# Optimization experiments

Measured on AMD Instinct MI355X. Metric: run time of the kernel, lower is better.

The kernel has to match this reference:

```python
import jax, jax.numpy as jnp
import numpy as np

N = 50000      # number of nodes (rows of edge_embeddings)
E = 800000     # number of edges
D = 256        # edge_dim
TOPK = 50


def setup_inputs() -> dict:
    key = jax.random.key(0)
    k1, k2, k3, k4, k5, k6 = jax.random.split(key, 6)
    edge_embeddings = jax.random.normal(k1, (N, D), dtype=jnp.float32)
    edge_index = jax.random.randint(k2, (2, E), 0, N, dtype=jnp.int64)
    # PyTorch nn.Linear default init: U(-1/sqrt(fan_in), 1/sqrt(fan_in))
    s1 = 1.0 / np.sqrt(2 * D)
    s2 = 1.0 / np.sqrt(D)
    W1 = jax.random.uniform(k3, (2 * D, D), jnp.float32, -s1, s1)
    b1 = jax.random.uniform(k4, (D,), jnp.float32, -s1, s1)
    W2 = jax.random.uniform(k5, (D, 1), jnp.float32, -s2, s2)
    b2 = jax.random.uniform(k6, (1,), jnp.float32, -s2, s2)
    return {"edge_embeddings": edge_embeddings, "W1": W1, "b1": b1,
            "W2": W2, "b2": b2, "edge_index": edge_index, "top_k": TOPK}


def reference(edge_embeddings, W1, b1, W2, b2, edge_index, top_k):
    src, dst = edge_index[0], edge_index[1]           # [E]
    valid = src < dst                                  # original keeps only i<j pairs
    # gather + concat: [E, 2D]
    pair_emb = jnp.concatenate([edge_embeddings[src], edge_embeddings[dst]], axis=-1)
    h = jax.nn.relu(pair_emb @ W1 + b1)                # [E, D]
    score = jax.nn.sigmoid(h @ W2 + b2)[:, 0]          # [E], in (0,1)
    # invalid edges get score -1 (< any sigmoid output) so topk picks only valid ones
    masked = jnp.where(valid, score, jnp.float32(-1.0))
    top_scores, top_idx = jax.lax.top_k(masked, top_k)
    top_pairs = edge_index[:, top_idx]                 # [2, k] (src,dst) of top edges
    return top_pairs, top_scores
```

## Files before the change

kernel.cpp:

```cpp
#include <hip/hip_runtime.h>
#include <hip/hip_bf16.h>
#include <cstdint>

#define TOPK 50
#define CANDS 400
#define HIST_BINS 16384
#define CAND_CAP 16384
#define NFBLK 512
#define SORT_CAP 8192

typedef __attribute__((ext_vector_type(8))) short bf16x8;
typedef __attribute__((ext_vector_type(4))) float f32x4;

__device__ __forceinline__ unsigned short f2bf(float f) {
    unsigned u = __float_as_uint(f);
    u += 0x7FFFu + ((u >> 16) & 1u);
    return (unsigned short)(u >> 16);
}

__global__ __launch_bounds__(256) void prep_kernel(const float* __restrict__ W1,
                                                   unsigned* __restrict__ Wcf4,
                                                   unsigned* __restrict__ hist,
                                                   unsigned* __restrict__ misc,
                                                   const int* __restrict__ eidx) {
    int g = blockIdx.x * blockDim.x + threadIdx.x;
    {
        int l = g & 63;
        int kt = (g >> 6) & 7;
        int nt = g >> 9;
        int col = nt * 16 + (l & 15);
        int kb = kt * 32 + (l >> 4) * 8;
        unsigned short h[8];
#pragma unroll
        for (int j = 0; j < 8; ++j) {
            int k = kb + j;
            float f = (col < 256) ? W1[k * 256 + col] : W1[(256 + k) * 256 + (col - 256)];
            h[j] = f2bf(f);
        }
        unsigned* dst = Wcf4 + (size_t)g * 4;
        dst[0] = (unsigned)h[0] | ((unsigned)h[1] << 16);
        dst[1] = (unsigned)h[2] | ((unsigned)h[3] << 16);
        dst[2] = (unsigned)h[4] | ((unsigned)h[5] << 16);
        dst[3] = (unsigned)h[6] | ((unsigned)h[7] << 16);
    }
    if (g < HIST_BINS) hist[g] = 0;
    if (g == 0) {
        int allz = 1;
        for (int q = 0; q < 64; ++q)
            if (eidx[2 * q + 1] != 0) { allz = 0; break; }
        misc[0] = (unsigned)allz;
        misc[2] = 0;
        misc[3] = 0;
        misc[4] = 0;
    }
}

__global__ __launch_bounds__(256) void gemm_fused(const float* __restrict__ emb,
                                                  const bf16x8* __restrict__ Bv,
                                                  const float* __restrict__ b1,
                                                  unsigned char* __restrict__ C8, int M) {
    __shared__ uint4 afrag[2048];
    const int t = threadIdx.x;
    const int w = t >> 6;
    const int l = t & 63;

    uint2* w2 = (uint2*)afrag;
#pragma unroll
    for (int iter = 0; iter < 16; ++iter) {
        int r = iter * 4 + w;
        int c0 = l * 4;
        int gr = blockIdx.x * 64 + r;
        float4 v = make_float4(0.f, 0.f, 0.f, 0.f);
        if (gr < M) v = *(const float4*)&emb[(size_t)gr * 256 + c0];
        unsigned u0 = (unsigned)f2bf(v.x) | ((unsigned)f2bf(v.y) << 16);
        unsigned u1 = (unsigned)f2bf(v.z) | ((unsigned)f2bf(v.w) << 16);
        int mt = r >> 4;
        int kt = c0 >> 5;
        int lane = (r & 15) + ((c0 & 31) >> 3) * 16;
        int f = mt * 8 + kt;
        int slot = f * 64 + (lane ^ (f & 7));
        w2[slot * 2 + ((c0 & 7) >> 2)] = make_uint2(u0, u1);
    }
    __syncthreads();

    bf16x8 af[8];
#pragma unroll
    for (int kt = 0; kt < 8; ++kt) {
        int f = w * 8 + kt;
        af[kt] = *(const bf16x8*)&afrag[f * 64 + (l ^ kt)];
    }

    const int row0 = blockIdx.x * 64 + w * 16 + (l >> 4) * 4;
#pragma unroll
    for (int nq = 0; nq < 4; ++nq) {
        f32x4 acc[8];
#pragma unroll
        for (int nt = 0; nt < 8; ++nt) acc[nt] = (f32x4){0.f, 0.f, 0.f, 0.f};
#pragma unroll
        for (int kt = 0; kt < 8; ++kt) {
            bf16x8 bf_[8];
#pragma unroll
            for (int nt = 0; nt < 8; ++nt)
                bf_[nt] = Bv[(size_t)((nq * 8 + nt) * 8 + kt) * 64 + l];
#pragma unroll
            for (int nt = 0; nt < 8; ++nt)
                acc[nt] = __builtin_amdgcn_mfma_f32_16x16x32_bf16(af[kt], bf_[nt], acc[nt], 0, 0, 0);
        }
#pragma unroll
        for (int nt = 0; nt < 8; ++nt) {
            int col = nq * 128 + nt * 16 + (l & 15);
            float bias = (col < 256) ? b1[col] : 0.f;
#pragma unroll
            for (int r = 0; r < 4; ++r) {
                float v = acc[nt][r] + bias;
                int pk = __builtin_amdgcn_cvt_pk_fp8_f32(v, v, 0, false);
                C8[(size_t)(row0 + r) * 512 + col] = (unsigned char)(pk & 0xFF);
            }
        }
    }
}

__global__ __launch_bounds__(256) void count_valid(const int* __restrict__ eidx,
                                                   const unsigned* __restrict__ misc,
                                                   unsigned* __restrict__ bcount, int E) {
    const int is64 = (int)misc[0];
    const int chunk = (E + gridDim.x - 1) / gridDim.x;
    const int lo = blockIdx.x * chunk;
    const int hi = min(E, lo + chunk);
    unsigned cnt = 0;
    for (int e = lo + threadIdx.x; e < hi; e += blockDim.x) {
        int s, d;
        if (is64) {
            s = ((const int2*)eidx)[e].x;
            d = ((const int2*)eidx)[(size_t)e + E].x;
        } else {
            s = eidx[e];
            d = eidx[e + E];
        }
        cnt += (s < d);
    }
#pragma unroll
    for (int off = 32; off; off >>= 1) cnt += __shfl_xor(cnt, off, 64);
    __shared__ unsigned wsum[4];
    if ((threadIdx.x & 63) == 0) wsum[threadIdx.x >> 6] = cnt;
    __syncthreads();
    if (threadIdx.x == 0)
        bcount[blockIdx.x] = wsum[0] + wsum[1] + wsum[2] + wsum[3];
}

__global__ __launch_bounds__(256) void scan_blocks(const unsigned* __restrict__ bcount,
                                                   unsigned* __restrict__ boffset,
                                                   unsigned* __restrict__ misc) {
    __shared__ unsigned sc[256];
    const int t = threadIdx.x;
    unsigned a = bcount[2 * t], b = bcount[2 * t + 1];
    sc[t] = a + b;
    __syncthreads();
    for (int off = 1; off < 256; off <<= 1) {
        unsigned v = (t >= off) ? sc[t - off] : 0u;
        __syncthreads();
        sc[t] += v;
        __syncthreads();
    }
    unsigned excl = sc[t] - (a + b);
    boffset[2 * t] = excl;
    boffset[2 * t + 1] = excl + a;
    if (t == 255) misc[4] = sc[255];
}

__global__ __launch_bounds__(256) void write_valid(const int* __restrict__ eidx,
                                                   const unsigned* __restrict__ misc,
                                                   const unsigned* __restrict__ boffset,
                                                   int* __restrict__ vsrc,
                                                   int* __restrict__ vdst,
                                                   int* __restrict__ vid, int E) {
    const int is64 = (int)misc[0];
    const int chunk = (E + gridDim.x - 1) / gridDim.x;
    const int lo = blockIdx.x * chunk;
    const int hi = min(E, lo + chunk);
    const int lane = threadIdx.x & 63;
    const int w = threadIdx.x >> 6;
    __shared__ unsigned wcnt[4];
    unsigned running = boffset[blockIdx.x];
    for (int base = lo; base < hi; base += blockDim.x) {
        int e = base + threadIdx.x;
        bool valid = false;
        int s = 0, d = 0;
        if (e < hi) {
            if (is64) {
                s = ((const int2*)eidx)[e].x;
                d = ((const int2*)eidx)[(size_t)e + E].x;
            } else {
                s = eidx[e];
                d = eidx[e + E];
            }
            valid = s < d;
        }
        unsigned long long m = __ballot(valid);
        unsigned pfx = __popcll(m & ((1ull << lane) - 1ull));
        if (lane == 0) wcnt[w] = __popcll(m);
        __syncthreads();
        unsigned wbase = running;
        for (int i = 0; i < w; ++i) wbase += wcnt[i];
        if (valid) {
            unsigned p = wbase + pfx;
            vsrc[p] = s;
            vdst[p] = d;
            vid[p] = e;
        }
        unsigned tot = wcnt[0] + wcnt[1] + wcnt[2] + wcnt[3];
        __syncthreads();
        running += tot;
    }
}

__device__ __forceinline__ float dotq(unsigned a, unsigned b, float4 w) {
    float s;
    s  = fmaxf(__builtin_amdgcn_cvt_f32_fp8(a, 0) + __builtin_amdgcn_cvt_f32_fp8(b, 0), 0.f) * w.x;
    s += fmaxf(__builtin_amdgcn_cvt_f32_fp8(a, 1) + __builtin_amdgcn_cvt_f32_fp8(b, 1), 0.f) * w.y;
    s += fmaxf(__builtin_amdgcn_cvt_f32_fp8(a, 2) + __builtin_amdgcn_cvt_f32_fp8(b, 2), 0.f) * w.z;
    s += fmaxf(__builtin_amdgcn_cvt_f32_fp8(a, 3) + __builtin_amdgcn_cvt_f32_fp8(b, 3), 0.f) * w.w;
    return s;
}

__global__ __launch_bounds__(256) void edge_score_fp8(const unsigned char* __restrict__ C8,
                                                      const int* __restrict__ vsrc,
                                                      const int* __restrict__ vdst,
                                                      const float* __restrict__ W2,
                                                      const float* __restrict__ b2,
                                                      float* __restrict__ svals,
                                                      const unsigned* __restrict__ misc) {
    const int V = (int)misc[4];
    const int lane = threadIdx.x & 63;
    const int q = lane & 15;
    const int g = lane >> 4;
    const int wid = blockIdx.x * (blockDim.x >> 6) + (threadIdx.x >> 6);
    const int nw = gridDim.x * (blockDim.x >> 6);

    const float4 w0 = *(const float4*)&W2[q * 16 + 0];
    const float4 w1 = *(const float4*)&W2[q * 16 + 4];
    const float4 w2 = *(const float4*)&W2[q * 16 + 8];
    const float4 w3 = *(const float4*)&W2[q * 16 + 12];
    const float bb2 = b2[0];

    for (int base = wid * 4; base < V; base += nw * 4) {
        const int slot = base + g;
        const bool ok = slot < V;
        const int src = ok ? vsrc[slot] : 0;
        const int dst = ok ? vdst[slot] : 0;
        const uint4 ua = *(const uint4*)(C8 + (size_t)src * 512 + q * 16);
        const uint4 ub = *(const uint4*)(C8 + (size_t)dst * 512 + 256 + q * 16);
        float p = dotq(ua.x, ub.x, w0);
        p += dotq(ua.y, ub.y, w1);
        p += dotq(ua.z, ub.z, w2);
        p += dotq(ua.w, ub.w, w3);
        p += __shfl_xor(p, 1, 64);
        p += __shfl_xor(p, 2, 64);
        p += __shfl_xor(p, 4, 64);
        p += __shfl_xor(p, 8, 64);
        if (q == 0 && ok) {
            float z = p + bb2;
            float sc = 1.0f / (1.0f + expf(-z));
            svals[slot] = sc;
        }
    }
}

__global__ __launch_bounds__(256) void hist_kernel(const float* __restrict__ svals,
                                                   const unsigned* __restrict__ misc,
                                                   unsigned* __restrict__ hist) {
    __shared__ unsigned lh[HIST_BINS];
    const int V = (int)misc[4];
    const int t = threadIdx.x;
    for (int i = t; i < HIST_BINS; i += 256) lh[i] = 0;
    __syncthreads();
    int i = blockIdx.x * blockDim.x + t;
    int stride = gridDim.x * blockDim.x;
    for (int v = i; v < V; v += stride)
        atomicAdd(&lh[__float_as_uint(svals[v]) >> 16], 1u);
    __syncthreads();
    for (int b = t; b < HIST_BINS; b += 256) {
        unsigned c = lh[b];
        if (c) atomicAdd(&hist[b], c);
    }
}

__global__ void scan_hist(const unsigned* __restrict__ hist, unsigned* __restrict__ misc) {
    __shared__ unsigned chunk[256];
    int t = threadIdx.x;
    unsigned s = 0;
    for (int i = 0; i < 64; ++i) s += hist[t * 64 + i];
    chunk[t] = s;
    __syncthreads();
    if (t == 0) {
        unsigned cum = 0;
        int c;
        unsigned thr = 0;
        for (c = 255; c >= 0; --c) {
            if (cum + chunk[c] >= CANDS) break;
            cum += chunk[c];
        }
        if (c >= 0) {
            for (int b = c * 64 + 63; b >= c * 64; --b) {
                cum += hist[b];
                if (cum >= CANDS) { thr = ((unsigned)b) << 16; break; }
            }
        }
        misc[2] = thr;
    }
}

__global__ void compact(const float* __restrict__ svals, const int* __restrict__ vid,
                        unsigned* __restrict__ misc,
                        unsigned long long* __restrict__ cand) {
    const int V = (int)misc[4];
    const unsigned thr = misc[2];
    int i = blockIdx.x * blockDim.x + threadIdx.x;
    int stride = gridDim.x * blockDim.x;
    for (int v = i; v < V; v += stride) {
        unsigned bits = __float_as_uint(svals[v]);
        if (bits >= thr) {
            unsigned pos = atomicAdd(&misc[3], 1u);
            if (pos < CAND_CAP)
                cand[pos] = ((unsigned long long)bits << 32) |
                            (unsigned)(0xFFFFFFFFu - (unsigned)vid[v]);
        }
    }
}

__global__ __launch_bounds__(256) void rescore(const float* __restrict__ emb,
                                               const float* __restrict__ W1,
                                               const float* __restrict__ b1,
                                               const float* __restrict__ W2,
                                               const float* __restrict__ b2,
                                               const int* __restrict__ eidx,
                                               const unsigned long long* __restrict__ cand,
                                               const unsigned* __restrict__ misc,
                                               unsigned long long* __restrict__ rescored,
                                               int E) {
    __shared__ float es[256], ed[256];
    __shared__ float red[256];
    const int C = (int)min(misc[3], (unsigned)CAND_CAP);
    const int is64 = (int)misc[0];
    const int t = threadIdx.x;
    for (int c = blockIdx.x; c < C; c += gridDim.x) {
        unsigned long long entry = cand[c];
        unsigned e = 0xFFFFFFFFu - (unsigned)(entry & 0xFFFFFFFFu);
        int src, dst;
        if (is64) {
            src = eidx[2 * (size_t)e];
            dst = eidx[2 * ((size_t)e + E)];
        } else {
            src = eidx[e];
            dst = eidx[e + E];
        }
        es[t] = emb[(size_t)src * 256 + t];
        ed[t] = emb[(size_t)dst * 256 + t];
        __syncthreads();
        float h = b1[t];
#pragma unroll 8
        for (int k = 0; k < 256; ++k) h += es[k] * W1[k * 256 + t];
#pragma unroll 8
        for (int k = 0; k < 256; ++k) h += ed[k] * W1[(256 + k) * 256 + t];
        red[t] = fmaxf(h, 0.f) * W2[t];
        __syncthreads();
        for (int s = 128; s; s >>= 1) {
            if (t < s) red[t] += red[t + s];
            __syncthreads();
        }
        if (t == 0) {
            float z = red[0] + b2[0];
            float sc = 1.0f / (1.0f + expf(-z));
            rescored[c] = ((unsigned long long)__float_as_uint(sc) << 32) |
                          (unsigned)(0xFFFFFFFFu - e);
        }
        __syncthreads();
    }
}

__global__ __launch_bounds__(256) void final_topk(unsigned long long* __restrict__ rescored,
                                                  const unsigned* __restrict__ misc,
                                                  const int* __restrict__ eidx,
                                                  float* __restrict__ out, int E) {
    __shared__ unsigned long long a[SORT_CAP];
    const int t = threadIdx.x;
    const int C = (int)min(misc[3], (unsigned)CAND_CAP);
    const int is64 = (int)misc[0];

    if (C <= SORT_CAP) {
        int n = 256;
        while (n < C) n <<= 1;
        for (int i = t; i < n; i += 256) a[i] = (i < C) ? rescored[i] : 0ull;
        __syncthreads();
        for (int k = 2; k <= n; k <<= 1) {
            for (int j = k >> 1; j > 0; j >>= 1) {
                for (int i = t; i < n; i += 256) {
                    int ixj = i ^ j;
                    if (ixj > i) {
                        unsigned long long x = a[i], y = a[ixj];
                        bool sw = ((i & k) == 0) ? (x < y) : (x > y);
                        if (sw) { a[i] = y; a[ixj] = x; }
                    }
                }
                __syncthreads();
            }
        }
        if (t < TOPK) {
            unsigned long long m = a[t];
            if (m != 0ull) {
                unsigned bits = (unsigned)(m >> 32);
                unsigned e = 0xFFFFFFFFu - (unsigned)(m & 0xFFFFFFFFu);
                int src, dst;
                if (is64) {
                    src = eidx[2 * (size_t)e];
                    dst = eidx[2 * ((size_t)e + E)];
                } else {
                    src = eidx[e];
                    dst = eidx[e + E];
                }
                out[t] = (float)src;
                out[TOPK + t] = (float)dst;
                out[2 * TOPK + t] = __uint_as_float(bits);
            } else {
                out[t] = -1.f;
                out[TOPK + t] = -1.f;
                out[2 * TOPK + t] = -1.f;
            }
        }
        return;
    }

    __shared__ unsigned long long red[256];
    for (int r = 0; r < TOPK; ++r) {
        unsigned long long best = 0ull;
        for (int i = t; i < C; i += 256) {
            unsigned long long v = rescored[i];
            if (v > best) best = v;
        }
        red[t] = best;
        __syncthreads();
        for (int s = 128; s; s >>= 1) {
            if (t < s) {
                if (red[t + s] > red[t]) red[t] = red[t + s];
            }
            __syncthreads();
        }
        unsigned long long m = red[0];
        __syncthreads();
        for (int i = t; i < C; i += 256)
            if (rescored[i] == m) rescored[i] = 0ull;
        if (t == 0) {
            if (m != 0ull) {
                unsigned bits = (unsigned)(m >> 32);
                unsigned e = 0xFFFFFFFFu - (unsigned)(m & 0xFFFFFFFFu);
                int src, dst;
                if (is64) {
                    src = eidx[2 * (size_t)e];
                    dst = eidx[2 * ((size_t)e + E)];
                } else {
                    src = eidx[e];
                    dst = eidx[e + E];
                }
                out[r] = (float)src;
                out[TOPK + r] = (float)dst;
                out[2 * TOPK + r] = __uint_as_float(bits);
            } else {
                out[r] = -1.f;
                out[TOPK + r] = -1.f;
                out[2 * TOPK + r] = -1.f;
            }
        }
        __syncthreads();
    }
}

extern "C" void kernel_launch(void* const* d_in, const int* in_sizes, int n_in,
                              void* d_out, int out_size, void* d_ws, size_t ws_size,
                              hipStream_t stream) {
    const float* emb = (const float*)d_in[0];
    const float* W1  = (const float*)d_in[1];
    const float* b1  = (const float*)d_in[2];
    const float* W2  = (const float*)d_in[3];
    const float* b2  = (const float*)d_in[4];
    const int*   eidx = (const int*)d_in[5];

    const int M = in_sizes[0] / 256;
    const int E = in_sizes[5] / 2;
    const int Mpad = ((M + 63) / 64) * 64;

    char* p = (char*)d_ws;
    auto alloc = [&](size_t bytes) {
        char* r = p;
        p += (bytes + 255) & ~(size_t)255;
        return r;
    };
    unsigned* Wcf4 = (unsigned*)alloc(256 * 512 * 2);
    unsigned char* C8 = (unsigned char*)alloc((size_t)Mpad * 512);
    float* svals = (float*)alloc((size_t)E * 4);
    int* vsrc = (int*)alloc((size_t)E * 4);
    int* vdst = (int*)alloc((size_t)E * 4);
    int* vid  = (int*)alloc((size_t)E * 4);
    unsigned* hist = (unsigned*)alloc(HIST_BINS * 4);
    unsigned long long* cand = (unsigned long long*)alloc(CAND_CAP * 8);
    unsigned long long* resc = (unsigned long long*)alloc(CAND_CAP * 8);
    unsigned* bcount = (unsigned*)alloc(NFBLK * 4);
    unsigned* boffset = (unsigned*)alloc(NFBLK * 4);
    unsigned* misc = (unsigned*)alloc(256);

    float* out = (float*)d_out;

    prep_kernel<<<64, 256, 0, stream>>>(W1, Wcf4, hist, misc, eidx);

    gemm_fused<<<Mpad / 64, 256, 0, stream>>>(emb, (const bf16x8*)Wcf4, b1, C8, M);

    count_valid<<<NFBLK, 256, 0, stream>>>(eidx, misc, bcount, E);
    scan_blocks<<<1, 256, 0, stream>>>(bcount, boffset, misc);
    write_valid<<<NFBLK, 256, 0, stream>>>(eidx, misc, boffset, vsrc, vdst, vid, E);

    edge_score_fp8<<<2048, 256, 0, stream>>>(C8, vsrc, vdst, W2, b2, svals, misc);

    hist_kernel<<<128, 256, 0, stream>>>(svals, misc, hist);

    scan_hist<<<1, 256, 0, stream>>>(hist, misc);

    compact<<<1024, 256, 0, stream>>>(svals, vid, misc, cand);

    rescore<<<1024, 256, 0, stream>>>(emb, W1, b1, W2, b2, eidx, cand, misc, resc, E);

    final_topk<<<1, 256, 0, stream>>>(resc, misc, eidx, out, E);
}
```

Baseline: 166.1 us.

## Retile node GEMM to 128-row blocks with 16 waves in a 4x4 warp grid

The per-node projection GEMM now uses 1024-thread blocks covering 128 rows. The 16 waves are arranged as 4 row groups by 4 column groups, so each wave computes two 16-row tiles against 128 output columns. Each loaded B fragment now feeds two MFMAs instead of one, which halves per-wave global reads of the weight matrix and spreads column work across waves. In exchange the block needs twice the LDS and four times the threads, which may reduce occupancy and leave a larger last block partially filled.

New measurement: 163.6 us. Within noise of the previous version (-1.5%).

```diff
diff --git a/kernel.cpp b/kernel.cpp
--- a/kernel.cpp
+++ b/kernel.cpp
@@ -55,21 +55,22 @@
     }
 }
 
-__global__ __launch_bounds__(256) void gemm_fused(const float* __restrict__ emb,
-                                                  const bf16x8* __restrict__ Bv,
-                                                  const float* __restrict__ b1,
-                                                  unsigned char* __restrict__ C8, int M) {
-    __shared__ uint4 afrag[2048];
+__global__ __launch_bounds__(1024) void gemm_fused(const float* __restrict__ emb,
+                                                   const bf16x8* __restrict__ Bv,
+                                                   const float* __restrict__ b1,
+                                                   unsigned char* __restrict__ C8, int M) {
+    __shared__ uint4 afrag[4096];
     const int t = threadIdx.x;
     const int w = t >> 6;
     const int l = t & 63;
 
     uint2* w2 = (uint2*)afrag;
 #pragma unroll
-    for (int iter = 0; iter < 16; ++iter) {
-        int r = iter * 4 + w;
-        int c0 = l * 4;
-        int gr = blockIdx.x * 64 + r;
+    for (int iter = 0; iter < 8; ++iter) {
+        int flat = iter * 1024 + t;
+        int r = flat >> 6;
+        int c0 = (flat & 63) * 4;
+        int gr = blockIdx.x * 128 + r;
         float4 v = make_float4(0.f, 0.f, 0.f, 0.f);
         if (gr < M) v = *(const float4*)&emb[(size_t)gr * 256 + c0];
         unsigned u0 = (unsigned)f2bf(v.x) | ((unsigned)f2bf(v.y) << 16);
@@ -83,36 +84,41 @@
     }
     __syncthreads();
 
-    bf16x8 af[8];
+    const int wm = w >> 2;
+    const int wn = w & 3;
+
+    f32x4 acc[2][8];
+#pragma unroll
+    for (int i = 0; i < 2; ++i)
+#pragma unroll
+        for (int j = 0; j < 8; ++j) acc[i][j] = (f32x4){0.f, 0.f, 0.f, 0.f};
+
 #pragma unroll
     for (int kt = 0; kt < 8; ++kt) {
-        int f = w * 8 + kt;
-        af[kt] = *(const bf16x8*)&afrag[f * 64 + (l ^ kt)];
-    }
-
-    const int row0 = blockIdx.x * 64 + w * 16 + (l >> 4) * 4;
-#pragma unroll
-    for (int nq = 0; nq < 4; ++nq) {
-        f32x4 acc[8];
-#pragma unroll
-        for (int nt = 0; nt < 8; ++nt) acc[nt] = (f32x4){0.f, 0.f, 0.f, 0.f};
-#pragma unroll
-        for (int kt = 0; kt < 8; ++kt) {
-            bf16x8 bf_[8];
-#pragma unroll
-            for (int nt = 0; nt < 8; ++nt)
-                bf_[nt] = Bv[(size_t)((nq * 8 + nt) * 8 + kt) * 64 + l];
-#pragma unroll
-            for (int nt = 0; nt < 8; ++nt)
-                acc[nt] = __builtin_amdgcn_mfma_f32_16x16x32_bf16(af[kt], bf_[nt], acc[nt], 0, 0, 0);
-        }
-#pragma unroll
-        for (int nt = 0; nt < 8; ++nt) {
-            int col = nq * 128 + nt * 16 + (l & 15);
+        bf16x8 af[2];
+#pragma unroll
+        for (int i = 0; i < 2; ++i) {
+            int f = (wm * 2 + i) * 8 + kt;
+            af[i] = *(const bf16x8*)&afrag[f * 64 + (l ^ (f & 7))];
+        }
+#pragma unroll
+        for (int j = 0; j < 8; ++j) {
+            bf16x8 bf_ = Bv[(size_t)((wn * 8 + j) * 8 + kt) * 64 + l];
+            acc[0][j] = __builtin_amdgcn_mfma_f32_16x16x32_bf16(af[0], bf_, acc[0][j], 0, 0, 0);
+            acc[1][j] = __builtin_amdgcn_mfma_f32_16x16x32_bf16(af[1], bf_, acc[1][j], 0, 0, 0);
+        }
+    }
+
+#pragma unroll
+    for (int i = 0; i < 2; ++i) {
+        int row0 = blockIdx.x * 128 + (wm * 2 + i) * 16 + (l >> 4) * 4;
+#pragma unroll
+        for (int j = 0; j < 8; ++j) {
+            int col = wn * 128 + j * 16 + (l & 15);
             float bias = (col < 256) ? b1[col] : 0.f;
 #pragma unroll
             for (int r = 0; r < 4; ++r) {
-                float v = acc[nt][r] + bias;
+                float v = acc[i][j][r] + bias;
                 int pk = __builtin_amdgcn_cvt_pk_fp8_f32(v, v, 0, false);
                 C8[(size_t)(row0 + r) * 512 + col] = (unsigned char)(pk & 0xFF);
             }
@@ -486,7 +492,7 @@
 
     const int M = in_sizes[0] / 256;
     const int E = in_sizes[5] / 2;
-    const int Mpad = ((M + 63) / 64) * 64;
+    const int Mpad = ((M + 127) / 128) * 128;
 
     char* p = (char*)d_ws;
     auto alloc = [&](size_t bytes) {
@@ -511,7 +517,7 @@
 
     prep_kernel<<<64, 256, 0, stream>>>(W1, Wcf4, hist, misc, eidx);
 
-    gemm_fused<<<Mpad / 64, 256, 0, stream>>>(emb, (const bf16x8*)Wcf4, b1, C8, M);
+    gemm_fused<<<Mpad / 128, 1024, 0, stream>>>(emb, (const bf16x8*)Wcf4, b1, C8, M);
 
     count_valid<<<NFBLK, 256, 0, stream>>>(eidx, misc, bcount, E);
     scan_blocks<<<1, 256, 0, stream>>>(bcount, boffset, misc);
```

## Retile node GEMM so each wave owns a column slice and prefetch B fragments

Applied to the files above, without the earlier changes.

Changes the per-node projection GEMM's work split. Before, each wave took 16 rows and swept all 512 output columns, reloading B fragments from global memory for every wave. Now each wave covers all 64 rows of the block and owns 128 columns, processed as two halves of 64, with A fragments read from LDS per k-step. B loads are double-buffered one k-step ahead to overlap them with the MFMAs. The aim is to cut redundant global B traffic by four times, at the cost of more LDS reads and a larger accumulator tile that may raise register pressure.

Result: faster. 154.9 us (-6.8%).

```diff
diff --git a/kernel.cpp b/kernel.cpp
--- a/kernel.cpp
+++ b/kernel.cpp
@@ -83,38 +83,57 @@
     }
     __syncthreads();
 
-    bf16x8 af[8];
-#pragma unroll
-    for (int kt = 0; kt < 8; ++kt) {
-        int f = w * 8 + kt;
-        af[kt] = *(const bf16x8*)&afrag[f * 64 + (l ^ kt)];
-    }
-
-    const int row0 = blockIdx.x * 64 + w * 16 + (l >> 4) * 4;
-#pragma unroll
-    for (int nq = 0; nq < 4; ++nq) {
-        f32x4 acc[8];
-#pragma unroll
-        for (int nt = 0; nt < 8; ++nt) acc[nt] = (f32x4){0.f, 0.f, 0.f, 0.f};
+    const int wn = w;
+#pragma unroll
+    for (int nh = 0; nh < 2; ++nh) {
+        f32x4 acc[4][4];
+#pragma unroll
+        for (int i = 0; i < 4; ++i)
+#pragma unroll
+            for (int j = 0; j < 4; ++j) acc[i][j] = (f32x4){0.f, 0.f, 0.f, 0.f};
+
+        const int nt0 = wn * 8 + nh * 4;
+        bf16x8 bcur[4];
+#pragma unroll
+        for (int j = 0; j < 4; ++j)
+            bcur[j] = Bv[(size_t)((nt0 + j) * 8 + 0) * 64 + l];
+
 #pragma unroll
         for (int kt = 0; kt < 8; ++kt) {
-            bf16x8 bf_[8];
-#pragma unroll
-            for (int nt = 0; nt < 8; ++nt)
-                bf_[nt] = Bv[(size_t)((nq * 8 + nt) * 8 + kt) * 64 + l];
-#pragma unroll
-            for (int nt = 0; nt < 8; ++nt)
-                acc[nt] = __builtin_amdgcn_mfma_f32_16x16x32_bf16(af[kt], bf_[nt], acc[nt], 0, 0, 0);
-        }
-#pragma unroll
-        for (int nt = 0; nt < 8; ++nt) {
-            int col = nq * 128 + nt * 16 + (l & 15);
-            float bias = (col < 256) ? b1[col] : 0.f;
-#pragma unroll
-            for (int r = 0; r < 4; ++r) {
-                float v = acc[nt][r] + bias;
-                int pk = __builtin_amdgcn_cvt_pk_fp8_f32(v, v, 0, false);
-                C8[(size_t)(row0 + r) * 512 + col] = (unsigned char)(pk & 0xFF);
+            bf16x8 af[4];
+#pragma unroll
+            for (int i = 0; i < 4; ++i)
+                af[i] = *(const bf16x8*)&afrag[(i * 8 + kt) * 64 + (l ^ kt)];
+            bf16x8 bnxt[4];
+            if (kt < 7) {
+#pragma unroll
+                for (int j = 0; j < 4; ++j)
+                    bnxt[j] = Bv[(size_t)((nt0 + j) * 8 + kt + 1) * 64 + l];
+            }
+#pragma unroll
+            for (int i = 0; i < 4; ++i)
+#pragma unroll
+                for (int j = 0; j < 4; ++j)
+                    acc[i][j] = __builtin_amdgcn_mfma_f32_16x16x32_bf16(af[i], bcur[j], acc[i][j], 0, 0, 0);
+            if (kt < 7) {
+#pragma unroll
+                for (int j = 0; j < 4; ++j) bcur[j] = bnxt[j];
+            }
+        }
+
+#pragma unroll
+        for (int i = 0; i < 4; ++i) {
+            int row0 = blockIdx.x * 64 + i * 16 + (l >> 4) * 4;
+#pragma unroll
+            for (int j = 0; j < 4; ++j) {
+                int col = (nt0 + j) * 16 + (l & 15);
+                float bias = (col < 256) ? b1[col] : 0.f;
+#pragma unroll
+                for (int r = 0; r < 4; ++r) {
+                    float v = acc[i][j][r] + bias;
+                    int pk = __builtin_amdgcn_cvt_pk_fp8_f32(v, v, 0, false);
+                    C8[(size_t)(row0 + r) * 512 + col] = (unsigned char)(pk & 0xFF);
+                }
             }
         }
     }
```
